# Kernel tuning notes

Measured on AMD Instinct MI355X. Metric: run time of the kernel, lower is better.

## Reference

```python
import jax, jax.numpy as jnp
import numpy as np

B, L, D, H = 4, 1024, 256, 8
TEMP = float(np.sqrt(D))
EPS_SM = 1e-6
EPS_LN = 1e-5


def setup_inputs() -> dict:
    key = jax.random.key(0)
    ks = jax.random.split(key, 8)
    std = float(np.sqrt(2.0 / (D * 2)))
    return {
        "q": jax.random.normal(ks[0], (B, L, D), jnp.float32),
        "mask": jax.random.randint(ks[1], (B, L, L), 0, 2, jnp.int32),
        "k": jax.random.normal(ks[2], (B, L, D), jnp.float32),
        "v": jax.random.normal(ks[3], (B, L, D), jnp.float32),
        "w_qs": jax.random.normal(ks[4], (H * D, D), jnp.float32) * std,
        "w_ks": jax.random.normal(ks[5], (H * D, D), jnp.float32) * std,
        "w_vs": jax.random.normal(ks[6], (H * D, D), jnp.float32) * std,
        "fc_w": jax.random.normal(ks[7], (D, H * D), jnp.float32) * float(np.sqrt(2.0 / (D + H * D))),
        "fc_b": jnp.zeros((D,), jnp.float32),
        "ln_g": jnp.ones((D,), jnp.float32),
        "ln_b": jnp.zeros((D,), jnp.float32),
    }


def masked_softmax(x, m):
    # repo's layers.masked_softmax: clamp, mask-mul, stable exp, mask-mul, normalize
    x = jnp.clip(x, -15.0, 15.0) * m
    e = jnp.exp(x - jnp.max(x, axis=-1, keepdims=True)) * m
    return e / (jnp.sum(e, axis=-1, keepdims=True) + EPS_SM)


def reference(q, mask, k, v, w_qs, w_ks, w_vs, fc_w, fc_b, ln_g, ln_b):
    residual = q
    m = mask.astype(q.dtype)[:, None, :, :]          # [B,1,Lq,Lk]
    # projections to per-head full-dim: [B,L,H,D]
    qh = (q @ w_qs.T).reshape(B, L, H, D)
    kh = (k @ w_ks.T).reshape(B, L, H, D)
    vh = (v @ w_vs.T).reshape(B, L, H, D)
    scores = jnp.einsum("bqhd,bkhd->bhqk", qh, kh) / TEMP   # [B,H,Lq,Lk]
    attn = masked_softmax(scores, m)
    out = jnp.einsum("bhqk,bkhd->bqhd", attn, vh).reshape(B, L, H * D)
    out = out @ fc_w.T + fc_b                         # [B,L,D]
    out = out + residual
    mu = jnp.mean(out, axis=-1, keepdims=True)
    var = jnp.var(out, axis=-1, keepdims=True)
    out = (out - mu) / jnp.sqrt(var + EPS_LN) * ln_g + ln_b
    # match torch attn layout: [H*B, Lq, Lk] (head-major)
    attn_hb = jnp.transpose(attn, (1, 0, 2, 3)).reshape(H * B, L, L)
    return out, attn_hb
```

## Files before the change

### kernel.cpp

```cpp
#include <hip/hip_runtime.h>
#include <cstdint>
#include <math.h>

#define Bsz 4
#define Lsz 1024
#define Dsz 256
#define Hsz 8
#define HD  2048
#define NROWS (Bsz*Lsz)
#define INV_TEMP 0.0625f

typedef __attribute__((ext_vector_type(8))) short bf16x8;
typedef __attribute__((ext_vector_type(4))) float f32x4;

__device__ inline unsigned short f2bf(float f) {
    union { float f; unsigned u; } x; x.f = f;
    unsigned r = x.u + 0x7fffu + ((x.u >> 16) & 1u);
    return (unsigned short)(r >> 16);
}
__device__ inline float bf2f(unsigned short u) {
    union { unsigned u; float f; } x; x.u = (unsigned)u << 16; return x.f;
}

#define GBL(p) ((const __attribute__((address_space(1))) unsigned int*)(p))
#define LDS(p) ((__attribute__((address_space(3))) unsigned int*)(p))

template <int TMv, int TNv, typename OutT, int EPI, int MINW>
__global__ __launch_bounds__(256, MINW) void gemm_bt(
    const unsigned short* __restrict__ A, const unsigned short* __restrict__ Bm,
    OutT* __restrict__ C,
    int K, int lda, int ldb, int ldc, int inner,
    long long sA1, long long sA2, long long sB1, long long sB2,
    long long sC1, long long sC2, float alpha,
    const int* __restrict__ mask, long long sM2,
    const float* __restrict__ invs, long long sI1, long long sI2)
{
    constexpr int WMv = TMv / 2, WNv = TNv / 2;
    constexpr int IT = TMv / 32, JT = TNv / 32;
    constexpr int APASS = TMv / 32, NPASS = (TMv + TNv) / 32;

    const int z  = blockIdx.z;
    const int i1 = z / inner;
    const int i2 = z % inner;
    A  += (size_t)i1 * sA1 + (size_t)i2 * sA2;
    Bm += (size_t)i1 * sB1 + (size_t)i2 * sB2;
    C  += (size_t)i1 * sC1 + (size_t)i2 * sC2;
    if (EPI == 1) mask += (size_t)i2 * sM2;
    if (EPI == 2) invs += (size_t)i1 * sI1 + (size_t)i2 * sI2;

    __shared__ unsigned short S[(TMv + TNv) * 64];
    unsigned short* As = S;
    unsigned short* Bs = S + TMv * 64;

    const int t    = threadIdx.x;
    const int lane = t & 63;
    const int w    = t >> 6;
    const int wm   = w & 1;
    const int wn   = w >> 1;
    const int m0   = blockIdx.x * TMv;
    const int n0   = blockIdx.y * TNv;

    const int rA = t >> 3;
    const int ch = (((t & 7) ^ (rA & 7))) * 8;
    const unsigned short* gA = A  + (size_t)(m0 + rA) * lda + ch;
    const unsigned short* gB = Bm + (size_t)(n0 + rA) * ldb + ch;

    const int fr = lane & 15;
    const int q  = lane >> 4;

    f32x4 acc[IT][JT];
#pragma unroll
    for (int i = 0; i < IT; ++i)
#pragma unroll
        for (int j = 0; j < JT; ++j) acc[i][j] = (f32x4){0.f, 0.f, 0.f, 0.f};

    for (int k0 = 0; k0 < K; k0 += 64) {
#pragma unroll
        for (int p = 0; p < NPASS; ++p) {
            const unsigned short* src = (p < APASS)
                ? (gA + (size_t)p * 32 * lda + k0)
                : (gB + (size_t)(p - APASS) * 32 * ldb + k0);
            __builtin_amdgcn_global_load_lds(GBL(src), LDS(S + p * 2048 + t * 8), 16, 0, 0);
        }
        __syncthreads();

#pragma unroll
        for (int ks = 0; ks < 2; ++ks) {
            const int slot = ((ks * 4 + q) ^ (fr & 7)) * 8;
            bf16x8 a[IT], b[JT];
#pragma unroll
            for (int i = 0; i < IT; ++i)
                a[i] = *(const bf16x8*)(As + (wm * WMv + i * 16 + fr) * 64 + slot);
#pragma unroll
            for (int j = 0; j < JT; ++j)
                b[j] = *(const bf16x8*)(Bs + (wn * WNv + j * 16 + fr) * 64 + slot);
#pragma unroll
            for (int i = 0; i < IT; ++i)
#pragma unroll
                for (int j = 0; j < JT; ++j)
                    acc[i][j] = __builtin_amdgcn_mfma_f32_16x16x32_bf16(a[i], b[j], acc[i][j], 0, 0, 0);
        }
        __syncthreads();
    }

#pragma unroll
    for (int i = 0; i < IT; ++i) {
#pragma unroll
        for (int r = 0; r < 4; ++r) {
            const int row = m0 + wm * WMv + i * 16 + q * 4 + r;
#pragma unroll
            for (int j = 0; j < JT; ++j) {
                const int col = n0 + wn * WNv + j * 16 + fr;
                float vv = acc[i][j][r] * alpha;
                if (EPI == 0) {
                    if constexpr (sizeof(OutT) == 4)
                        C[(size_t)row * ldc + col] = (OutT)vv;
                    else
                        ((unsigned short*)C)[(size_t)row * ldc + col] = f2bf(vv);
                } else if (EPI == 1) {
                    const float m = (float)mask[(size_t)row * Lsz + col];
                    vv = fminf(fmaxf(vv, -15.f), 15.f) * m;
                    vv = __expf(vv) * m;
                    ((unsigned short*)C)[(size_t)row * ldc + col] = f2bf(vv);
                } else {
                    vv *= invs[row];
                    ((unsigned short*)C)[(size_t)row * ldc + col] = f2bf(vv);
                }
            }
        }
    }
}

__global__ __launch_bounds__(256) void cast_all(
    const float* __restrict__ q, const float* __restrict__ k, const float* __restrict__ v,
    const float* __restrict__ wq, const float* __restrict__ wk, const float* __restrict__ wv,
    const float* __restrict__ fw,
    unsigned short* __restrict__ qb, unsigned short* __restrict__ kb, unsigned short* __restrict__ vb,
    unsigned short* __restrict__ wqb, unsigned short* __restrict__ wkb, unsigned short* __restrict__ wvb,
    unsigned short* __restrict__ fwb)
{
    const int gid = blockIdx.x * 256 + threadIdx.x;
    const int NQ = 262144;
    const int NW = 131072;
    const float* src; unsigned short* dst; int off;
    if      (gid < NQ)            { src = q;  dst = qb;  off = gid; }
    else if (gid < 2 * NQ)        { src = k;  dst = kb;  off = gid - NQ; }
    else if (gid < 3 * NQ)        { src = v;  dst = vb;  off = gid - 2 * NQ; }
    else if (gid < 3 * NQ + NW)   { src = wq; dst = wqb; off = gid - 3 * NQ; }
    else if (gid < 3 * NQ + 2*NW) { src = wk; dst = wkb; off = gid - 3 * NQ - NW; }
    else if (gid < 3 * NQ + 3*NW) { src = wv; dst = wvb; off = gid - 3 * NQ - 2 * NW; }
    else                          { src = fw; dst = fwb; off = gid - 3 * NQ - 3 * NW; }
    float4 f = ((const float4*)src)[off];
    ushort4 o;
    o.x = f2bf(f.x); o.y = f2bf(f.y); o.z = f2bf(f.z); o.w = f2bf(f.w);
    ((ushort4*)dst)[off] = o;
}

__global__ __launch_bounds__(256) void norm_kernel(const unsigned short* __restrict__ e,
                                                   float* __restrict__ attn,
                                                   float* __restrict__ invsum)
{
    const int r    = blockIdx.x * 4 + (threadIdx.x >> 6);
    const int lane = threadIdx.x & 63;
    const unsigned short* rowp = e + (size_t)r * Lsz + lane * 16;

    union { uint4 v[2]; unsigned short u[16]; } buf;
    buf.v[0] = *(const uint4*)rowp;
    buf.v[1] = *(const uint4*)(rowp + 8);

    float f[16];
    float s = 0.f;
#pragma unroll
    for (int i = 0; i < 16; ++i) { f[i] = bf2f(buf.u[i]); s += f[i]; }
#pragma unroll
    for (int o = 1; o <= 32; o <<= 1) s += __shfl_xor(s, o, 64);
    const float inv = 1.0f / (s + 1e-6f);

    float* op = attn + (size_t)r * Lsz + lane * 16;
#pragma unroll
    for (int c = 0; c < 4; ++c) {
        float4 o4;
        o4.x = f[c * 4 + 0] * inv; o4.y = f[c * 4 + 1] * inv;
        o4.z = f[c * 4 + 2] * inv; o4.w = f[c * 4 + 3] * inv;
        *(float4*)(op + c * 4) = o4;
    }
    if (lane == 0) invsum[r] = inv;
}

__global__ __launch_bounds__(256) void ln_kernel(const float* __restrict__ gout,
                                                 const float* __restrict__ qin,
                                                 const float* __restrict__ fc_b,
                                                 const float* __restrict__ ln_g,
                                                 const float* __restrict__ ln_b,
                                                 float* __restrict__ out)
{
    const int row = blockIdx.x;
    const int t = threadIdx.x;
    const size_t idx = (size_t)row * Dsz + t;
    const size_t P = (size_t)NROWS * Dsz;
    const float val = gout[idx] + gout[idx + P] + gout[idx + 2 * P] + gout[idx + 3 * P]
                    + fc_b[t] + qin[idx];

    __shared__ float red[4];
    float s = val;
#pragma unroll
    for (int o = 32; o > 0; o >>= 1) s += __shfl_down(s, o, 64);
    const int lane = t & 63, w = t >> 6;
    if (lane == 0) red[w] = s;
    __syncthreads();
    const float mu = (red[0] + red[1] + red[2] + red[3]) * (1.0f / Dsz);
    __syncthreads();

    float d = val - mu;
    float s2 = d * d;
#pragma unroll
    for (int o = 32; o > 0; o >>= 1) s2 += __shfl_down(s2, o, 64);
    if (lane == 0) red[w] = s2;
    __syncthreads();
    const float var = (red[0] + red[1] + red[2] + red[3]) * (1.0f / Dsz);

    out[idx] = d * rsqrtf(var + 1e-5f) * ln_g[t] + ln_b[t];
}

extern "C" void kernel_launch(void* const* d_in, const int* in_sizes, int n_in,
                              void* d_out, int out_size, void* d_ws, size_t ws_size,
                              hipStream_t stream)
{
    const float* q    = (const float*)d_in[0];
    const int*   mask = (const int*)d_in[1];
    const float* k    = (const float*)d_in[2];
    const float* v    = (const float*)d_in[3];
    const float* w_qs = (const float*)d_in[4];
    const float* w_ks = (const float*)d_in[5];
    const float* w_vs = (const float*)d_in[6];
    const float* fc_w = (const float*)d_in[7];
    const float* fc_b = (const float*)d_in[8];
    const float* ln_g = (const float*)d_in[9];
    const float* ln_b = (const float*)d_in[10];

    float* out  = (float*)d_out;
    float* attn = (float*)d_out + (size_t)NROWS * Dsz;

    unsigned short* wsu = (unsigned short*)d_ws;
    unsigned short* qh     = wsu;
    unsigned short* kh     = qh + (size_t)NROWS * HD;
    unsigned short* q_bf   = kh + (size_t)NROWS * HD;
    unsigned short* k_bf   = q_bf + (size_t)NROWS * Dsz;
    unsigned short* v_bf   = k_bf + (size_t)NROWS * Dsz;
    unsigned short* wq_bf  = v_bf + (size_t)NROWS * Dsz;
    unsigned short* wk_bf  = wq_bf + (size_t)HD * Dsz;
    unsigned short* wv_bf  = wk_bf + (size_t)HD * Dsz;
    unsigned short* vt     = wv_bf + (size_t)HD * Dsz;
    unsigned short* attn_e = vt + (size_t)Bsz * HD * Lsz;
    unsigned short* attnv  = attn_e + (size_t)32 * Lsz * Lsz;
    unsigned short* fcw_bf = attnv + (size_t)NROWS * HD;
    float*          invsum = (float*)(fcw_bf + (size_t)Dsz * HD);
    float*          fcout  = invsum + 32768;

    dim3 blk(256);

    cast_all<<<dim3(5120), blk, 0, stream>>>(q, k, v, w_qs, w_ks, w_vs, fc_w,
                                             q_bf, k_bf, v_bf, wq_bf, wk_bf, wv_bf, fcw_bf);

    {
        dim3 grid(NROWS / 64, HD / 256, 2);
        gemm_bt<64, 256, unsigned short, 0, 3><<<grid, blk, 0, stream>>>(q_bf, wq_bf, qh,
            Dsz, Dsz, Dsz, HD, 2,
            0, (long long)NROWS * Dsz, 0, (long long)HD * Dsz, 0, (long long)NROWS * HD,
            1.0f, nullptr, 0, nullptr, 0, 0);
    }

    {
        dim3 grid(HD / 64, Lsz / 256, Bsz);
        gemm_bt<64, 256, unsigned short, 0, 3><<<grid, blk, 0, stream>>>(wv_bf, v_bf, vt,
            Dsz, Dsz, Dsz, Lsz, 1,
            0, 0, (long long)Lsz * Dsz, 0, (long long)HD * Lsz, 0,
            1.0f, nullptr, 0, nullptr, 0, 0);
    }

    {
        dim3 grid(Lsz / 128, Lsz / 256, Hsz * Bsz);
        gemm_bt<128, 256, unsigned short, 1, 2><<<grid, blk, 0, stream>>>(qh, kh, attn_e,
            Dsz, HD, HD, Lsz, Bsz,
            Dsz, (long long)Lsz * HD, Dsz, (long long)Lsz * HD,
            (long long)Bsz * Lsz * Lsz, (long long)Lsz * Lsz,
            INV_TEMP, mask, (long long)Lsz * Lsz, nullptr, 0, 0);
    }

    norm_kernel<<<dim3(32 * Lsz / 4), blk, 0, stream>>>(attn_e, attn, invsum);

    {
        dim3 grid(Lsz / 64, Dsz / 256, Hsz * Bsz);
        gemm_bt<64, 256, unsigned short, 2, 3><<<grid, blk, 0, stream>>>(attn_e, vt, attnv,
            Lsz, Lsz, Lsz, HD, Bsz,
            (long long)Bsz * Lsz * Lsz, (long long)Lsz * Lsz,
            (long long)Dsz * Lsz, (long long)HD * Lsz,
            Dsz, (long long)Lsz * HD,
            1.0f, nullptr, 0, invsum, (long long)Bsz * Lsz, (long long)Lsz);
    }

    {
        dim3 grid(NROWS / 64, Dsz / 256, 4);
        gemm_bt<64, 256, float, 0, 3><<<grid, blk, 0, stream>>>(attnv, fcw_bf, fcout,
            512, HD, HD, Dsz, 4,
            0, 512, 0, 512, 0, (long long)NROWS * Dsz,
            1.0f, nullptr, 0, nullptr, 0, 0);
    }

    ln_kernel<<<dim3(NROWS), blk, 0, stream>>>(fcout, q, fc_b, ln_g, ln_b, out);
}
```

Baseline: 348.2 us.

## Stage bf16 GEMM epilogue through LDS and merge Q/K/V projection launches

Refactors the GEMM into a device body. For bf16 outputs it stages results through shared memory and writes them back as coalesced 16-byte row stores, replacing the scattered 2-byte stores. It merges the Q/K and V projection GEMMs into one launch and sets all GEMM variants to a uniform min-waves launch bound of 2. Staging adds extra barriers and LDS traffic in the epilogue, and the lower occupancy hint for the small-tile kernels may change register allocation.

```diff
diff --git a/kernel.cpp b/kernel.cpp
--- a/kernel.cpp
+++ b/kernel.cpp
@@ -25,8 +25,131 @@
 #define GBL(p) ((const __attribute__((address_space(1))) unsigned int*)(p))
 #define LDS(p) ((__attribute__((address_space(3))) unsigned int*)(p))
 
-template <int TMv, int TNv, typename OutT, int EPI, int MINW>
-__global__ __launch_bounds__(256, MINW) void gemm_bt(
+template <int TMv, int TNv, typename OutT, int EPI>
+__device__ __forceinline__ void gemm_body(
+    const unsigned short* __restrict__ A, const unsigned short* __restrict__ Bm,
+    OutT* __restrict__ C, int K, int lda, int ldb, int ldc,
+    int m0, int n0, float alpha,
+    const int* __restrict__ mask, const float* __restrict__ invs,
+    unsigned short* S)
+{
+    constexpr int WMv = TMv / 2, WNv = TNv / 2;
+    constexpr int IT = TMv / 32, JT = TNv / 32;
+    constexpr int APASS = TMv / 32, NPASS = (TMv + TNv) / 32;
+
+    unsigned short* As = S;
+    unsigned short* Bs = S + TMv * 64;
+
+    const int t    = threadIdx.x;
+    const int lane = t & 63;
+    const int w    = t >> 6;
+    const int wm   = w & 1;
+    const int wn   = w >> 1;
+
+    const int rA = t >> 3;
+    const int ch = (((t & 7) ^ (rA & 7))) * 8;
+    const unsigned short* gA = A  + (size_t)(m0 + rA) * lda + ch;
+    const unsigned short* gB = Bm + (size_t)(n0 + rA) * ldb + ch;
+
+    const int fr = lane & 15;
+    const int q  = lane >> 4;
+
+    f32x4 acc[IT][JT];
+#pragma unroll
+    for (int i = 0; i < IT; ++i)
+#pragma unroll
+        for (int j = 0; j < JT; ++j) acc[i][j] = (f32x4){0.f, 0.f, 0.f, 0.f};
+
+    for (int k0 = 0; k0 < K; k0 += 64) {
+#pragma unroll
+        for (int p = 0; p < NPASS; ++p) {
+            const unsigned short* src = (p < APASS)
+                ? (gA + (size_t)p * 32 * lda + k0)
+                : (gB + (size_t)(p - APASS) * 32 * ldb + k0);
+            __builtin_amdgcn_global_load_lds(GBL(src), LDS(S + p * 2048 + t * 8), 16, 0, 0);
+        }
+        __syncthreads();
+
+#pragma unroll
+        for (int ks = 0; ks < 2; ++ks) {
+            const int slot = ((ks * 4 + q) ^ (fr & 7)) * 8;
+            bf16x8 a[IT], b[JT];
+#pragma unroll
+            for (int i = 0; i < IT; ++i)
+                a[i] = *(const bf16x8*)(As + (wm * WMv + i * 16 + fr) * 64 + slot);
+#pragma unroll
+            for (int j = 0; j < JT; ++j)
+                b[j] = *(const bf16x8*)(Bs + (wn * WNv + j * 16 + fr) * 64 + slot);
+#pragma unroll
+            for (int i = 0; i < IT; ++i)
+#pragma unroll
+                for (int j = 0; j < JT; ++j)
+                    acc[i][j] = __builtin_amdgcn_mfma_f32_16x16x32_bf16(a[i], b[j], acc[i][j], 0, 0, 0);
+        }
+        __syncthreads();
+    }
+
+    constexpr bool BF16OUT = (EPI != 0) || (sizeof(OutT) == 2);
+    if constexpr (BF16OUT) {
+        constexpr int HALVES = TMv / 64;
+        unsigned short* T = S;
+#pragma unroll
+        for (int hm = 0; hm < HALVES; ++hm) {
+            if (HALVES == 1 || wm == hm) {
+#pragma unroll
+                for (int i = 0; i < IT; ++i) {
+#pragma unroll
+                    for (int r = 0; r < 4; ++r) {
+                        const int rl = (HALVES == 1 ? wm * WMv : 0) + i * 16 + q * 4 + r;
+                        const int grow = m0 + (HALVES == 1 ? 0 : hm * 64) + rl;
+#pragma unroll
+                        for (int j = 0; j < JT; ++j) {
+                            const int col = wn * WNv + j * 16 + fr;
+                            float vv = acc[i][j][r] * alpha;
+                            if (EPI == 1) {
+                                const float m = (float)mask[(size_t)grow * Lsz + (n0 + col)];
+                                vv = fminf(fmaxf(vv, -15.f), 15.f) * m;
+                                vv = __expf(vv) * m;
+                            } else if (EPI == 2) {
+                                vv *= invs[grow];
+                            }
+                            T[rl * TNv + col] = f2bf(vv);
+                        }
+                    }
+                }
+            }
+            __syncthreads();
+            constexpr int ROWB = TNv * 2;
+            constexpr int ITERS = (64 * TNv * 2) / (256 * 16);
+#pragma unroll
+            for (int it = 0; it < ITERS; ++it) {
+                const int off = t * 16 + it * 4096;
+                const int rl  = off / ROWB;
+                const int ce  = (off % ROWB) / 2;
+                uint4 d = *(const uint4*)((const char*)T + off);
+                const int grow = m0 + (HALVES == 1 ? 0 : hm * 64) + rl;
+                *(uint4*)((unsigned short*)C + (size_t)grow * ldc + (n0 + ce)) = d;
+            }
+            __syncthreads();
+        }
+    } else {
+#pragma unroll
+        for (int i = 0; i < IT; ++i) {
+#pragma unroll
+            for (int r = 0; r < 4; ++r) {
+                const int row = m0 + wm * WMv + i * 16 + q * 4 + r;
+#pragma unroll
+                for (int j = 0; j < JT; ++j) {
+                    const int col = n0 + wn * WNv + j * 16 + fr;
+                    C[(size_t)row * ldc + col] = (OutT)(acc[i][j][r] * alpha);
+                }
+            }
+        }
+    }
+}
+
+template <int TMv, int TNv, typename OutT, int EPI>
+__global__ __launch_bounds__(256, 2) void gemm_bt(
     const unsigned short* __restrict__ A, const unsigned short* __restrict__ Bm,
     OutT* __restrict__ C,
     int K, int lda, int ldb, int ldc, int inner,
@@ -35,10 +158,7 @@
     const int* __restrict__ mask, long long sM2,
     const float* __restrict__ invs, long long sI1, long long sI2)
 {
-    constexpr int WMv = TMv / 2, WNv = TNv / 2;
-    constexpr int IT = TMv / 32, JT = TNv / 32;
-    constexpr int APASS = TMv / 32, NPASS = (TMv + TNv) / 32;
-
+    __shared__ unsigned short S[(TMv + TNv) * 64];
     const int z  = blockIdx.z;
     const int i1 = z / inner;
     const int i2 = z % inner;
@@ -47,87 +167,38 @@
     C  += (size_t)i1 * sC1 + (size_t)i2 * sC2;
     if (EPI == 1) mask += (size_t)i2 * sM2;
     if (EPI == 2) invs += (size_t)i1 * sI1 + (size_t)i2 * sI2;
-
-    __shared__ unsigned short S[(TMv + TNv) * 64];
-    unsigned short* As = S;
-    unsigned short* Bs = S + TMv * 64;
-
-    const int t    = threadIdx.x;
-    const int lane = t & 63;
-    const int w    = t >> 6;
-    const int wm   = w & 1;
-    const int wn   = w >> 1;
-    const int m0   = blockIdx.x * TMv;
-    const int n0   = blockIdx.y * TNv;
-
-    const int rA = t >> 3;
-    const int ch = (((t & 7) ^ (rA & 7))) * 8;
-    const unsigned short* gA = A  + (size_t)(m0 + rA) * lda + ch;
-    const unsigned short* gB = Bm + (size_t)(n0 + rA) * ldb + ch;
-
-    const int fr = lane & 15;
-    const int q  = lane >> 4;
-
-    f32x4 acc[IT][JT];
-#pragma unroll
-    for (int i = 0; i < IT; ++i)
-#pragma unroll
-        for (int j = 0; j < JT; ++j) acc[i][j] = (f32x4){0.f, 0.f, 0.f, 0.f};
-
-    for (int k0 = 0; k0 < K; k0 += 64) {
-#pragma unroll
-        for (int p = 0; p < NPASS; ++p) {
-            const unsigned short* src = (p < APASS)
-                ? (gA + (size_t)p * 32 * lda + k0)
-                : (gB + (size_t)(p - APASS) * 32 * ldb + k0);
-            __builtin_amdgcn_global_load_lds(GBL(src), LDS(S + p * 2048 + t * 8), 16, 0, 0);
-        }
-        __syncthreads();
-
-#pragma unroll
-        for (int ks = 0; ks < 2; ++ks) {
-            const int slot = ((ks * 4 + q) ^ (fr & 7)) * 8;
-            bf16x8 a[IT], b[JT];
-#pragma unroll
-            for (int i = 0; i < IT; ++i)
-                a[i] = *(const bf16x8*)(As + (wm * WMv + i * 16 + fr) * 64 + slot);
-#pragma unroll
-            for (int j = 0; j < JT; ++j)
-                b[j] = *(const bf16x8*)(Bs + (wn * WNv + j * 16 + fr) * 64 + slot);
-#pragma unroll
-            for (int i = 0; i < IT; ++i)
-#pragma unroll
-                for (int j = 0; j < JT; ++j)
-                    acc[i][j] = __builtin_amdgcn_mfma_f32_16x16x32_bf16(a[i], b[j], acc[i][j], 0, 0, 0);
-        }
-        __syncthreads();
-    }
-
-#pragma unroll
-    for (int i = 0; i < IT; ++i) {
-#pragma unroll
-        for (int r = 0; r < 4; ++r) {
-            const int row = m0 + wm * WMv + i * 16 + q * 4 + r;
-#pragma unroll
-            for (int j = 0; j < JT; ++j) {
-                const int col = n0 + wn * WNv + j * 16 + fr;
-                float vv = acc[i][j][r] * alpha;
-                if (EPI == 0) {
-                    if constexpr (sizeof(OutT) == 4)
-                        C[(size_t)row * ldc + col] = (OutT)vv;
-                    else
-                        ((unsigned short*)C)[(size_t)row * ldc + col] = f2bf(vv);
-                } else if (EPI == 1) {
-                    const float m = (float)mask[(size_t)row * Lsz + col];
-                    vv = fminf(fmaxf(vv, -15.f), 15.f) * m;
-                    vv = __expf(vv) * m;
-                    ((unsigned short*)C)[(size_t)row * ldc + col] = f2bf(vv);
-                } else {
-                    vv *= invs[row];
-                    ((unsigned short*)C)[(size_t)row * ldc + col] = f2bf(vv);
-                }
-            }
-        }
+    gemm_body<TMv, TNv, OutT, EPI>(A, Bm, C, K, lda, ldb, ldc,
+        blockIdx.x * TMv, blockIdx.y * TNv, alpha, mask, invs, S);
+}
+
+__global__ __launch_bounds__(256, 2) void gemm_qkv(
+    const unsigned short* __restrict__ qb, const unsigned short* __restrict__ kb,
+    const unsigned short* __restrict__ vb,
+    const unsigned short* __restrict__ wq, const unsigned short* __restrict__ wk,
+    const unsigned short* __restrict__ wv,
+    unsigned short* __restrict__ qh, unsigned short* __restrict__ kh,
+    unsigned short* __restrict__ vt)
+{
+    __shared__ unsigned short S[(64 + 256) * 64];
+    const int bid = blockIdx.x;
+    if (bid < 1024) {
+        const int job = bid >> 9;
+        const int lx  = bid & 511;
+        const int m0  = (lx & 63) * 64;
+        const int n0  = ((lx >> 6) & 7) * 256;
+        const unsigned short* A = job ? kb : qb;
+        const unsigned short* B = job ? wk : wq;
+        unsigned short* C = job ? kh : qh;
+        gemm_body<64, 256, unsigned short, 0>(A, B, C, Dsz, Dsz, Dsz, HD,
+            m0, n0, 1.0f, nullptr, nullptr, S);
+    } else {
+        const int lx = bid - 1024;
+        const int m0 = (lx & 31) * 64;
+        const int n0 = ((lx >> 5) & 3) * 256;
+        const int b  = lx >> 7;
+        gemm_body<64, 256, unsigned short, 0>(wv, vb + (size_t)b * Lsz * Dsz,
+            vt + (size_t)b * HD * Lsz, Dsz, Dsz, Dsz, Lsz,
+            m0, n0, 1.0f, nullptr, nullptr, S);
     }
 }
 
@@ -262,25 +333,12 @@
     cast_all<<<dim3(5120), blk, 0, stream>>>(q, k, v, w_qs, w_ks, w_vs, fc_w,
                                              q_bf, k_bf, v_bf, wq_bf, wk_bf, wv_bf, fcw_bf);
 
-    {
-        dim3 grid(NROWS / 64, HD / 256, 2);
-        gemm_bt<64, 256, unsigned short, 0, 3><<<grid, blk, 0, stream>>>(q_bf, wq_bf, qh,
-            Dsz, Dsz, Dsz, HD, 2,
-            0, (long long)NROWS * Dsz, 0, (long long)HD * Dsz, 0, (long long)NROWS * HD,
-            1.0f, nullptr, 0, nullptr, 0, 0);
-    }
-
-    {
-        dim3 grid(HD / 64, Lsz / 256, Bsz);
-        gemm_bt<64, 256, unsigned short, 0, 3><<<grid, blk, 0, stream>>>(wv_bf, v_bf, vt,
-            Dsz, Dsz, Dsz, Lsz, 1,
-            0, 0, (long long)Lsz * Dsz, 0, (long long)HD * Lsz, 0,
-            1.0f, nullptr, 0, nullptr, 0, 0);
-    }
+    gemm_qkv<<<dim3(1536), blk, 0, stream>>>(q_bf, k_bf, v_bf, wq_bf, wk_bf, wv_bf,
+                                             qh, kh, vt);
 
     {
         dim3 grid(Lsz / 128, Lsz / 256, Hsz * Bsz);
-        gemm_bt<128, 256, unsigned short, 1, 2><<<grid, blk, 0, stream>>>(qh, kh, attn_e,
+        gemm_bt<128, 256, unsigned short, 1><<<grid, blk, 0, stream>>>(qh, kh, attn_e,
             Dsz, HD, HD, Lsz, Bsz,
             Dsz, (long long)Lsz * HD, Dsz, (long long)Lsz * HD,
             (long long)Bsz * Lsz * Lsz, (long long)Lsz * Lsz,
@@ -291,7 +349,7 @@
 
     {
         dim3 grid(Lsz / 64, Dsz / 256, Hsz * Bsz);
-        gemm_bt<64, 256, unsigned short, 2, 3><<<grid, blk, 0, stream>>>(attn_e, vt, attnv,
+        gemm_bt<64, 256, unsigned short, 2><<<grid, blk, 0, stream>>>(attn_e, vt, attnv,
             Lsz, Lsz, Lsz, HD, Bsz,
             (long long)Bsz * Lsz * Lsz, (long long)Lsz * Lsz,
             (long long)Dsz * Lsz, (long long)HD * Lsz,
@@ -301,7 +359,7 @@
 
     {
         dim3 grid(NROWS / 64, Dsz / 256, 4);
-        gemm_bt<64, 256, float, 0, 3><<<grid, blk, 0, stream>>>(attnv, fcw_bf, fcout,
+        gemm_bt<64, 256, float, 0><<<grid, blk, 0, stream>>>(attnv, fcw_bf, fcout,
             512, HD, HD, Dsz, 4,
             0, 512, 0, 512, 0, (long long)NROWS * Dsz,
             1.0f, nullptr, 0, nullptr, 0, 0);
```

After: 351.8 us. No clear change (+1.0%).
